# Kernel tuning notes

Hardware: AMD Instinct MI355X
Metric: run time of the kernel (lower is better)

Reference implementation:

```python
import jax, jax.numpy as jnp
import numpy as np

BN_EPS = 1e-5
NUM_GRAPHS = 64


def setup_inputs() -> dict:
    key = jax.random.key(0)
    ks = jax.random.split(key, 10)
    N, F, H, E = 50000, 128, 256, 800000
    x = jax.random.normal(ks[0], (N, F), dtype=jnp.float32)
    edge_index = jax.random.randint(ks[1], (2, E), 0, N, dtype=jnp.int64)
    batch = jnp.sort(jax.random.randint(ks[2], (N,), 0, NUM_GRAPHS, dtype=jnp.int64))
    # Linear weights stored as [in, out]; y = z @ w + b (equivalent to torch Linear)
    w1_0 = jax.random.normal(ks[3], (F, H), dtype=jnp.float32) / np.sqrt(F)
    b1_0 = jnp.zeros((H,), jnp.float32)
    w2_0 = jax.random.normal(ks[4], (H, H), dtype=jnp.float32) / np.sqrt(H)
    b2_0 = jnp.zeros((H,), jnp.float32)
    g_0 = jnp.ones((H,), jnp.float32)
    be_0 = jnp.zeros((H,), jnp.float32)
    w1_r = jax.random.normal(ks[5], (3, H, H), dtype=jnp.float32) / np.sqrt(H)
    b1_r = jnp.zeros((3, H), jnp.float32)
    w2_r = jax.random.normal(ks[6], (3, H, H), dtype=jnp.float32) / np.sqrt(H)
    b2_r = jnp.zeros((3, H), jnp.float32)
    g_r = jnp.ones((3, H), jnp.float32)
    be_r = jnp.zeros((3, H), jnp.float32)
    return dict(x=x, edge_index=edge_index, batch=batch,
                w1_0=w1_0, b1_0=b1_0, w2_0=w2_0, b2_0=b2_0, g_0=g_0, be_0=be_0,
                w1_r=w1_r, b1_r=b1_r, w2_r=w2_r, b2_r=b2_r, g_r=g_r, be_r=be_r)


def _gin_layer(h, src, dst, n, w1, b1, w2, b2, g, be):
    # GINConv with eps=0: MLP(h_i + sum_{j->i} h_j), scatter-add over edges
    agg = jax.ops.segment_sum(h[src], dst, num_segments=n)  # [N, d]
    z = agg + h
    z = jnp.maximum(z @ w1 + b1, 0.0)
    z = z @ w2 + b2
    # BatchNorm1d over the node dimension (training-mode batch statistics)
    mu = jnp.mean(z, axis=0)
    var = jnp.var(z, axis=0)
    z = (z - mu) * jax.lax.rsqrt(var + BN_EPS) * g + be
    return jnp.maximum(z, 0.0)  # ReLU; dropout is identity in eval mode


def reference(x, edge_index, batch, w1_0, b1_0, w2_0, b2_0, g_0, be_0,
              w1_r, b1_r, w2_r, b2_r, g_r, be_r):
    src, dst = edge_index[0], edge_index[1]
    n = x.shape[0]
    h = _gin_layer(x, src, dst, n, w1_0, b1_0, w2_0, b2_0, g_0, be_0)
    for i in range(3):
        h = _gin_layer(h, src, dst, n, w1_r[i], b1_r[i], w2_r[i], b2_r[i], g_r[i], be_r[i])
    # global mean pool per graph id
    counts = jax.ops.segment_sum(jnp.ones((n,), h.dtype), batch, num_segments=NUM_GRAPHS)
    pooled = jax.ops.segment_sum(h, batch, num_segments=NUM_GRAPHS)
    return pooled / jnp.maximum(counts, 1.0)[:, None]
```

## Files before the change

kernel.cpp:

```cpp
#include <hip/hip_runtime.h>

typedef float  f32x4 __attribute__((ext_vector_type(4)));
typedef _Float16 half8 __attribute__((ext_vector_type(8)));
typedef _Float16 half4 __attribute__((ext_vector_type(4)));

#define BN_EPS 1e-5f
#define NGRAPH 64

struct PrepArgs {
    const float* src[8];
    _Float16*    dst[8];
    int          K[8];
};

__global__ void prep_weights(PrepArgs a) {
    int m = blockIdx.y;
    int K = a.K[m];
    int total = K << 8;
    int idx = blockIdx.x * blockDim.x + threadIdx.x;
    if (idx >= total) return;
    int n = idx / K;
    int k = idx - n * K;
    a.dst[m][idx] = (_Float16)a.src[m][(size_t)k * 256 + n];
}

__global__ void edge_count(const int* __restrict__ ei, int* __restrict__ cnt,
                           int* __restrict__ rank, int E) {
    int e = blockIdx.x * blockDim.x + threadIdx.x;
    if (e < E) rank[e] = atomicAdd(&cnt[ei[E + e]], 1);
}

__global__ void scan_p1(const int* __restrict__ cnt, int* __restrict__ part, int N) {
    __shared__ int lds[256];
    int idx = blockIdx.x * 256 + threadIdx.x;
    lds[threadIdx.x] = (idx < N) ? cnt[idx] : 0;
    __syncthreads();
    for (int d = 128; d > 0; d >>= 1) {
        if (threadIdx.x < d) lds[threadIdx.x] += lds[threadIdx.x + d];
        __syncthreads();
    }
    if (threadIdx.x == 0) part[blockIdx.x] = lds[0];
}

__global__ void scan_p2(int* __restrict__ part, int* __restrict__ off, int N, int nb) {
    __shared__ int lds[256];
    int t = threadIdx.x;
    int v = (t < nb) ? part[t] : 0;
    lds[t] = v;
    __syncthreads();
    for (int d = 1; d < 256; d <<= 1) {
        int a = (t >= d) ? lds[t - d] : 0;
        __syncthreads();
        lds[t] += a;
        __syncthreads();
    }
    if (t < nb) part[t] = lds[t] - v;
    if (t == nb - 1) off[N] = lds[t];
}

__global__ void scan_p3(const int* __restrict__ cnt, const int* __restrict__ part,
                        int* __restrict__ off, int N) {
    __shared__ int lds[256];
    int t = threadIdx.x;
    int idx = blockIdx.x * 256 + t;
    int v = (idx < N) ? cnt[idx] : 0;
    lds[t] = v;
    __syncthreads();
    for (int d = 1; d < 256; d <<= 1) {
        int a = (t >= d) ? lds[t - d] : 0;
        __syncthreads();
        lds[t] += a;
        __syncthreads();
    }
    if (idx < N) off[idx] = part[blockIdx.x] + lds[t] - v;
}

__global__ void edge_fill(const int* __restrict__ ei, const int* __restrict__ off,
                          const int* __restrict__ rank, int* __restrict__ csr_src, int E) {
    int e = blockIdx.x * blockDim.x + threadIdx.x;
    if (e >= E) return;
    csr_src[off[ei[E + e]] + rank[e]] = ei[e];
}

__global__ void gather_f32(const float* __restrict__ x, const int* __restrict__ off,
                           const int* __restrict__ srcs, _Float16* __restrict__ out, int N) {
    int wid = (blockIdx.x << 2) + (threadIdx.x >> 6);
    if (wid >= N) return;
    int lane = threadIdx.x & 63;
    int half = lane >> 5;
    int fb = (lane & 31) << 2;
    float acc[4] = {0.f, 0.f, 0.f, 0.f};
    int beg = off[wid], end = off[wid + 1];
    int e = beg + half;
    for (; e + 2 < end; e += 4) {
        int s0 = srcs[e], s1 = srcs[e + 2];
        f32x4 v0 = *(const f32x4*)(x + (size_t)s0 * 128 + fb);
        f32x4 v1 = *(const f32x4*)(x + (size_t)s1 * 128 + fb);
#pragma unroll
        for (int k = 0; k < 4; ++k) acc[k] += v0[k] + v1[k];
    }
    if (e < end) {
        int s0 = srcs[e];
        f32x4 v0 = *(const f32x4*)(x + (size_t)s0 * 128 + fb);
#pragma unroll
        for (int k = 0; k < 4; ++k) acc[k] += v0[k];
    }
    if (half == 0) {
        f32x4 v = *(const f32x4*)(x + (size_t)wid * 128 + fb);
#pragma unroll
        for (int k = 0; k < 4; ++k) acc[k] += v[k];
    }
#pragma unroll
    for (int k = 0; k < 4; ++k) acc[k] += __shfl_xor(acc[k], 32);
    if (half == 0) {
        half4 o;
#pragma unroll
        for (int k = 0; k < 4; ++k) o[k] = (_Float16)acc[k];
        *(half4*)(out + (size_t)wid * 128 + fb) = o;
    }
}

__global__ void gather_fused(const _Float16* __restrict__ z, const int* __restrict__ off,
                             const int* __restrict__ srcs, const float* __restrict__ stats,
                             const float* __restrict__ gam, const float* __restrict__ bet,
                             _Float16* __restrict__ out, int N, float invN) {
    int wid = (blockIdx.x << 2) + (threadIdx.x >> 6);
    if (wid >= N) return;
    int lane = threadIdx.x & 63;
    int half = lane >> 5;
    int fb = (lane & 31) << 3;
    float sc[8], tc[8];
#pragma unroll
    for (int k = 0; k < 8; ++k) {
        float mu = stats[fb + k] * invN;
        float var = stats[256 + fb + k] * invN - mu * mu;
        float s = gam[fb + k] * rsqrtf(var + BN_EPS);
        sc[k] = s;
        tc[k] = bet[fb + k] - mu * s;
    }
    float acc[8] = {0.f, 0.f, 0.f, 0.f, 0.f, 0.f, 0.f, 0.f};
    int beg = off[wid], end = off[wid + 1];
    int e = beg + half;
    for (; e + 2 < end; e += 4) {
        int s0 = srcs[e], s1 = srcs[e + 2];
        half8 v0 = *(const half8*)(z + (size_t)s0 * 256 + fb);
        half8 v1 = *(const half8*)(z + (size_t)s1 * 256 + fb);
#pragma unroll
        for (int k = 0; k < 8; ++k)
            acc[k] += fmaxf(fmaf((float)v0[k], sc[k], tc[k]), 0.f)
                    + fmaxf(fmaf((float)v1[k], sc[k], tc[k]), 0.f);
    }
    if (e < end) {
        int s0 = srcs[e];
        half8 v0 = *(const half8*)(z + (size_t)s0 * 256 + fb);
#pragma unroll
        for (int k = 0; k < 8; ++k)
            acc[k] += fmaxf(fmaf((float)v0[k], sc[k], tc[k]), 0.f);
    }
    if (half == 0) {
        half8 v = *(const half8*)(z + (size_t)wid * 256 + fb);
#pragma unroll
        for (int k = 0; k < 8; ++k)
            acc[k] += fmaxf(fmaf((float)v[k], sc[k], tc[k]), 0.f);
    }
#pragma unroll
    for (int k = 0; k < 8; ++k) acc[k] += __shfl_xor(acc[k], 32);
    if (half == 0) {
        half8 o;
#pragma unroll
        for (int k = 0; k < 8; ++k) o[k] = (_Float16)acc[k];
        *(half8*)(out + (size_t)wid * 256 + fb) = o;
    }
}

template <int K, int WITH_STATS>
__global__ __launch_bounds__(512, 2) void gemm_kernel(
    const _Float16* __restrict__ A, const _Float16* __restrict__ BT,
    const float* __restrict__ bias, _Float16* __restrict__ Y,
    _Float16* __restrict__ Z, float* __restrict__ stats, int M) {
    extern __shared__ _Float16 blds[];
    const int tid = threadIdx.x;
    const int colbase = blockIdx.y * 128;
    {
        int row = tid >> 2;
        int q = tid & 3;
        int kq = q * (K / 4);
        const _Float16* src = BT + (size_t)(colbase + row) * K + kq;
        _Float16* dst = blds + row * K;
        int sw = (row & 7) << 3;
#pragma unroll
        for (int c = 0; c < K / 4; c += 8)
            *(half8*)(dst + ((kq + c) ^ sw)) = *(const half8*)(src + c);
    }
    __syncthreads();

    const int lane = tid & 63;
    const int wave = tid >> 6;
    const int i = lane & 15;
    const int g = lane >> 4;
    const int rowbase = blockIdx.x * 128 + wave * 16;
    const int arow = min(rowbase + i, M - 1);

    half8 afrag[K / 32];
#pragma unroll
    for (int s = 0; s < K / 32; ++s)
        afrag[s] = *(const half8*)(A + (size_t)arow * K + s * 32 + g * 8);

    f32x4 acc[8];
#pragma unroll
    for (int t = 0; t < 8; ++t) acc[t] = (f32x4){0.f, 0.f, 0.f, 0.f};

    const int sw = (i & 7) << 3;
#pragma unroll
    for (int s = 0; s < K / 32; ++s) {
#pragma unroll
        for (int t = 0; t < 8; ++t) {
            half8 b = *(const half8*)(blds + (t * 16 + i) * K + ((s * 32 + g * 8) ^ sw));
            acc[t] = __builtin_amdgcn_mfma_f32_16x16x32_f16(afrag[s], b, acc[t], 0, 0, 0);
        }
    }

    const int rg = g * 4;
    if (WITH_STATS == 0) {
#pragma unroll
        for (int t = 0; t < 8; ++t) {
            int c = colbase + t * 16 + i;
            float bv = bias[c];
#pragma unroll
            for (int j = 0; j < 4; ++j) {
                int r = rowbase + rg + j;
                if (r < M) Y[(size_t)r * 256 + c] = (_Float16)fmaxf(acc[t][j] + bv, 0.f);
            }
        }
    } else {
        float* sred = (float*)blds;
        __syncthreads();
#pragma unroll
        for (int t = 0; t < 8; ++t) {
            int c = colbase + t * 16 + i;
            float bv = bias[c];
            float s1 = 0.f, s2 = 0.f;
#pragma unroll
            for (int j = 0; j < 4; ++j) {
                int r = rowbase + rg + j;
                if (r < M) {
                    float v = acc[t][j] + bv;
                    Z[(size_t)r * 256 + c] = (_Float16)v;
                    s1 += v;
                    s2 += v * v;
                }
            }
            s1 += __shfl_xor(s1, 16); s1 += __shfl_xor(s1, 32);
            s2 += __shfl_xor(s2, 16); s2 += __shfl_xor(s2, 32);
            if (g == 0) {
                sred[wave * 128 + t * 16 + i] = s1;
                sred[1024 + wave * 128 + t * 16 + i] = s2;
            }
        }
        __syncthreads();
        if (tid < 256) {
            int which = tid >> 7;
            int c = tid & 127;
            float s = 0.f;
#pragma unroll
            for (int w = 0; w < 8; ++w) s += sred[which * 1024 + w * 128 + c];
            atomicAdd(&stats[which * 256 + colbase + c], s);
        }
    }
}

__global__ void graph_bounds(const int* __restrict__ batch, int* __restrict__ gstart, int N) {
    int t = threadIdx.x;
    if (t > NGRAPH) return;
    if (t == NGRAPH) { gstart[t] = N; return; }
    int lo = 0, hi = N;
    while (lo < hi) { int m = (lo + hi) >> 1; if (batch[m] < t) lo = m + 1; else hi = m; }
    gstart[t] = lo;
}

#define PCHUNK 256
__global__ void pool_stage1(const _Float16* __restrict__ z, const int* __restrict__ batch,
                            const int* __restrict__ gstart, const float* __restrict__ stats,
                            const float* __restrict__ gam, const float* __restrict__ bet,
                            float* __restrict__ acc, int N, float invN) {
    __shared__ float lds[8 * 512];
    int c0 = blockIdx.x * PCHUNK;
    int cend = min(c0 + PCHUNK, N);
    int tid = threadIdx.x;
    int rowlane = tid >> 5;
    int fb = (tid & 31) << 3;
    float sc[8], tc[8];
#pragma unroll
    for (int k = 0; k < 8; ++k) {
        float mu = stats[fb + k] * invN;
        float var = stats[256 + fb + k] * invN - mu * mu;
        float s = gam[fb + k] * rsqrtf(var + BN_EPS);
        sc[k] = s;
        tc[k] = bet[fb + k] - mu * s;
    }
    int segs = c0;
    while (segs < cend) {
        int g = batch[segs];
        int sege = min(gstart[g + 1], cend);
        float a[8] = {0.f, 0.f, 0.f, 0.f, 0.f, 0.f, 0.f, 0.f};
        for (int r = segs + rowlane; r < sege; r += 16) {
            half8 v = *(const half8*)(z + (size_t)r * 256 + fb);
#pragma unroll
            for (int k = 0; k < 8; ++k)
                a[k] += fmaxf(fmaf((float)v[k], sc[k], tc[k]), 0.f);
        }
#pragma unroll
        for (int k = 0; k < 8; ++k) lds[k * 512 + tid] = a[k];
        __syncthreads();
#pragma unroll
        for (int d = 8; d > 0; d >>= 1) {
            if (rowlane < d) {
#pragma unroll
                for (int k = 0; k < 8; ++k)
                    lds[k * 512 + tid] += lds[k * 512 + tid + d * 32];
            }
            __syncthreads();
        }
        if (rowlane == 0) {
#pragma unroll
            for (int k = 0; k < 8; ++k)
                atomicAdd(&acc[g * 256 + fb + k], lds[k * 512 + tid]);
        }
        __syncthreads();
        segs = sege;
    }
}

__global__ void pool_finalize(const float* __restrict__ acc, const int* __restrict__ gstart,
                              float* __restrict__ out) {
    int i = blockIdx.x * 256 + threadIdx.x;
    int g = i >> 8;
    int c = gstart[g + 1] - gstart[g];
    out[i] = acc[i] / (float)(c > 0 ? c : 1);
}

extern "C" void kernel_launch(void* const* d_in, const int* in_sizes, int n_in,
                              void* d_out, int out_size, void* d_ws, size_t ws_size,
                              hipStream_t stream) {
    const float* x    = (const float*)d_in[0];
    const int*   ei   = (const int*)d_in[1];
    const int*   batch= (const int*)d_in[2];
    const float* w1_0 = (const float*)d_in[3];
    const float* b1_0 = (const float*)d_in[4];
    const float* w2_0 = (const float*)d_in[5];
    const float* b2_0 = (const float*)d_in[6];
    const float* g_0  = (const float*)d_in[7];
    const float* be_0 = (const float*)d_in[8];
    const float* w1_r = (const float*)d_in[9];
    const float* b1_r = (const float*)d_in[10];
    const float* w2_r = (const float*)d_in[11];
    const float* b2_r = (const float*)d_in[12];
    const float* g_r  = (const float*)d_in[13];
    const float* be_r = (const float*)d_in[14];

    const int N = in_sizes[0] / 128;
    const int E = in_sizes[1] / 2;

    char* p = (char*)d_ws;
    auto alloc = [&](size_t bytes) { char* r = p; p += (bytes + 255) & ~(size_t)255; return r; };
    float*    stats   = (float*)alloc(4 * 512 * sizeof(float));
    int*      part    = (int*)alloc(256 * sizeof(int));
    int*      off     = (int*)alloc((size_t)(N + 1) * sizeof(int));
    int*      cnt     = (int*)alloc((size_t)N * sizeof(int));
    int*      gstart  = (int*)alloc(65 * sizeof(int));
    float*    acc     = (float*)alloc(NGRAPH * 256 * sizeof(float));
    int*      rank    = (int*)alloc((size_t)E * sizeof(int));
    int*      csr_src = (int*)alloc((size_t)E * sizeof(int));
    _Float16* wT      = (_Float16*)alloc((size_t)491520 * sizeof(_Float16));
    _Float16* zin     = (_Float16*)alloc((size_t)N * 256 * sizeof(_Float16));
    _Float16* y       = (_Float16*)alloc((size_t)N * 256 * sizeof(_Float16));
    _Float16* z       = (_Float16*)alloc((size_t)N * 256 * sizeof(_Float16));

    hipMemsetAsync(stats, 0, 4 * 512 * sizeof(float), stream);
    hipMemsetAsync(cnt, 0, (size_t)N * sizeof(int), stream);
    hipMemsetAsync(acc, 0, NGRAPH * 256 * sizeof(float), stream);

    PrepArgs pa;
    pa.src[0] = w1_0;  pa.dst[0] = wT;           pa.K[0] = 128;
    pa.src[1] = w2_0;  pa.dst[1] = wT + 32768;   pa.K[1] = 256;
    for (int i = 0; i < 3; ++i) {
        pa.src[2 + i] = w1_r + (size_t)i * 65536; pa.dst[2 + i] = wT + 98304 + (size_t)i * 65536; pa.K[2 + i] = 256;
        pa.src[5 + i] = w2_r + (size_t)i * 65536; pa.dst[5 + i] = wT + 294912 + (size_t)i * 65536; pa.K[5 + i] = 256;
    }
    prep_weights<<<dim3(256, 8), 256, 0, stream>>>(pa);

    const int eb = (E + 255) / 256;
    const int nb = (N + 255) / 256;
    edge_count<<<eb, 256, 0, stream>>>(ei, cnt, rank, E);
    scan_p1<<<nb, 256, 0, stream>>>(cnt, part, N);
    scan_p2<<<1, 256, 0, stream>>>(part, off, N, nb);
    scan_p3<<<nb, 256, 0, stream>>>(cnt, part, off, N);
    edge_fill<<<eb, 256, 0, stream>>>(ei, off, rank, csr_src, E);
    graph_bounds<<<1, 128, 0, stream>>>(batch, gstart, N);

    const int gwb   = (N + 3) / 4;
    const dim3 gemmg((N + 127) / 128, 2);
    const float invN = 1.0f / (float)N;

    gather_f32<<<gwb, 256, 0, stream>>>(x, off, csr_src, zin, N);
    gemm_kernel<128, 0><<<gemmg, 512, 128 * 128 * 2, stream>>>(zin, wT, b1_0, y, nullptr, nullptr, N);
    gemm_kernel<256, 1><<<gemmg, 512, 128 * 256 * 2, stream>>>(y, wT + 32768, b2_0, nullptr, z, stats, N);

    const float* cur_stats = stats;
    const float* cur_g = g_0;
    const float* cur_be = be_0;
    for (int i = 0; i < 3; ++i) {
        gather_fused<<<gwb, 256, 0, stream>>>(z, off, csr_src, cur_stats, cur_g, cur_be, zin, N, invN);
        gemm_kernel<256, 0><<<gemmg, 512, 128 * 256 * 2, stream>>>(
            zin, wT + 98304 + (size_t)i * 65536, b1_r + i * 256, y, nullptr, nullptr, N);
        gemm_kernel<256, 1><<<gemmg, 512, 128 * 256 * 2, stream>>>(
            y, wT + 294912 + (size_t)i * 65536, b2_r + i * 256, nullptr, z, stats + (i + 1) * 512, N);
        cur_stats = stats + (i + 1) * 512;
        cur_g = g_r + i * 256;
        cur_be = be_r + i * 256;
    }

    pool_stage1<<<(N + PCHUNK - 1) / PCHUNK, 512, 0, stream>>>(
        z, batch, gstart, cur_stats, cur_g, cur_be, acc, N, invN);
    pool_finalize<<<NGRAPH, 256, 0, stream>>>(acc, gstart, (float*)d_out);
}
```

Before: 576.1 us.

## Fuse both MLP GEMMs per layer, cast input to fp16, use packed half BN

Replaces the two separate GEMM launches per layer with one kernel. It computes the first GEMM into LDS, applies bias and ReLU there, then does the second GEMM reading W2 straight from global memory, which removes the round trip of the intermediate y through HBM. Input x is cast to fp16 once so the first gather reads half the bytes. The fused gather's BN+ReLU now runs in packed fp16 with deeper unrolling. Risks include lower fp16 precision in the BN transform, W2 fragments reloaded from global or L2 by every wave, and 1024-thread blocks using 128KB of LDS, which limits occupancy.

```diff
diff --git a/kernel.cpp b/kernel.cpp
--- a/kernel.cpp
+++ b/kernel.cpp
@@ -24,6 +24,17 @@
     a.dst[m][idx] = (_Float16)a.src[m][(size_t)k * 256 + n];
 }
 
+__global__ void cast_x(const float* __restrict__ x, _Float16* __restrict__ o, int total) {
+    int i = (blockIdx.x * blockDim.x + threadIdx.x) << 3;
+    if (i >= total) return;
+    f32x4 a = *(const f32x4*)(x + i);
+    f32x4 b = *(const f32x4*)(x + i + 4);
+    half8 r;
+#pragma unroll
+    for (int k = 0; k < 4; ++k) { r[k] = (_Float16)a[k]; r[k + 4] = (_Float16)b[k]; }
+    *(half8*)(o + i) = r;
+}
+
 __global__ void edge_count(const int* __restrict__ ei, int* __restrict__ cnt,
                            int* __restrict__ rank, int E) {
     int e = blockIdx.x * blockDim.x + threadIdx.x;
@@ -82,41 +93,44 @@
     csr_src[off[ei[E + e]] + rank[e]] = ei[e];
 }
 
-__global__ void gather_f32(const float* __restrict__ x, const int* __restrict__ off,
-                           const int* __restrict__ srcs, _Float16* __restrict__ out, int N) {
+__global__ void gather0(const _Float16* __restrict__ x, const int* __restrict__ off,
+                        const int* __restrict__ srcs, _Float16* __restrict__ out, int N) {
     int wid = (blockIdx.x << 2) + (threadIdx.x >> 6);
     if (wid >= N) return;
     int lane = threadIdx.x & 63;
-    int half = lane >> 5;
-    int fb = (lane & 31) << 2;
-    float acc[4] = {0.f, 0.f, 0.f, 0.f};
-    int beg = off[wid], end = off[wid + 1];
-    int e = beg + half;
-    for (; e + 2 < end; e += 4) {
-        int s0 = srcs[e], s1 = srcs[e + 2];
-        f32x4 v0 = *(const f32x4*)(x + (size_t)s0 * 128 + fb);
-        f32x4 v1 = *(const f32x4*)(x + (size_t)s1 * 128 + fb);
-#pragma unroll
-        for (int k = 0; k < 4; ++k) acc[k] += v0[k] + v1[k];
+    int q = lane >> 4;
+    int fb = (lane & 15) << 3;
+    float acc[8] = {0.f, 0.f, 0.f, 0.f, 0.f, 0.f, 0.f, 0.f};
+    int end = off[wid + 1];
+    int e = off[wid] + q;
+    for (; e + 4 < end; e += 8) {
+        int s0 = srcs[e], s1 = srcs[e + 4];
+        half8 v0 = *(const half8*)(x + (size_t)s0 * 128 + fb);
+        half8 v1 = *(const half8*)(x + (size_t)s1 * 128 + fb);
+#pragma unroll
+        for (int k = 0; k < 8; ++k) acc[k] += (float)v0[k] + (float)v1[k];
     }
     if (e < end) {
         int s0 = srcs[e];
-        f32x4 v0 = *(const f32x4*)(x + (size_t)s0 * 128 + fb);
-#pragma unroll
-        for (int k = 0; k < 4; ++k) acc[k] += v0[k];
-    }
-    if (half == 0) {
-        f32x4 v = *(const f32x4*)(x + (size_t)wid * 128 + fb);
-#pragma unroll
-        for (int k = 0; k < 4; ++k) acc[k] += v[k];
-    }
-#pragma unroll
-    for (int k = 0; k < 4; ++k) acc[k] += __shfl_xor(acc[k], 32);
-    if (half == 0) {
-        half4 o;
-#pragma unroll
-        for (int k = 0; k < 4; ++k) o[k] = (_Float16)acc[k];
-        *(half4*)(out + (size_t)wid * 128 + fb) = o;
+        half8 v0 = *(const half8*)(x + (size_t)s0 * 128 + fb);
+#pragma unroll
+        for (int k = 0; k < 8; ++k) acc[k] += (float)v0[k];
+    }
+    if (q == 0) {
+        half8 v = *(const half8*)(x + (size_t)wid * 128 + fb);
+#pragma unroll
+        for (int k = 0; k < 8; ++k) acc[k] += (float)v[k];
+    }
+#pragma unroll
+    for (int k = 0; k < 8; ++k) {
+        acc[k] += __shfl_xor(acc[k], 16);
+        acc[k] += __shfl_xor(acc[k], 32);
+    }
+    if (q == 0) {
+        half8 o;
+#pragma unroll
+        for (int k = 0; k < 8; ++k) o[k] = (_Float16)acc[k];
+        *(half8*)(out + (size_t)wid * 128 + fb) = o;
     }
 }
 
@@ -127,45 +141,51 @@
     int wid = (blockIdx.x << 2) + (threadIdx.x >> 6);
     if (wid >= N) return;
     int lane = threadIdx.x & 63;
-    int half = lane >> 5;
+    int hf = lane >> 5;
     int fb = (lane & 31) << 3;
-    float sc[8], tc[8];
+    half8 sc8, tc8;
 #pragma unroll
     for (int k = 0; k < 8; ++k) {
         float mu = stats[fb + k] * invN;
         float var = stats[256 + fb + k] * invN - mu * mu;
         float s = gam[fb + k] * rsqrtf(var + BN_EPS);
-        sc[k] = s;
-        tc[k] = bet[fb + k] - mu * s;
-    }
+        sc8[k] = (_Float16)s;
+        tc8[k] = (_Float16)(bet[fb + k] - mu * s);
+    }
+    const half8 zero8 = {0, 0, 0, 0, 0, 0, 0, 0};
     float acc[8] = {0.f, 0.f, 0.f, 0.f, 0.f, 0.f, 0.f, 0.f};
-    int beg = off[wid], end = off[wid + 1];
-    int e = beg + half;
-    for (; e + 2 < end; e += 4) {
-        int s0 = srcs[e], s1 = srcs[e + 2];
+    int end = off[wid + 1];
+    int e = off[wid] + hf;
+    for (; e + 6 < end; e += 8) {
+        int s0 = srcs[e], s1 = srcs[e + 2], s2 = srcs[e + 4], s3 = srcs[e + 6];
         half8 v0 = *(const half8*)(z + (size_t)s0 * 256 + fb);
         half8 v1 = *(const half8*)(z + (size_t)s1 * 256 + fb);
+        half8 v2 = *(const half8*)(z + (size_t)s2 * 256 + fb);
+        half8 v3 = *(const half8*)(z + (size_t)s3 * 256 + fb);
+        half8 r0 = __builtin_elementwise_max(v0 * sc8 + tc8, zero8);
+        half8 r1 = __builtin_elementwise_max(v1 * sc8 + tc8, zero8);
+        half8 r2 = __builtin_elementwise_max(v2 * sc8 + tc8, zero8);
+        half8 r3 = __builtin_elementwise_max(v3 * sc8 + tc8, zero8);
 #pragma unroll
         for (int k = 0; k < 8; ++k)
-            acc[k] += fmaxf(fmaf((float)v0[k], sc[k], tc[k]), 0.f)
-                    + fmaxf(fmaf((float)v1[k], sc[k], tc[k]), 0.f);
-    }
-    if (e < end) {
+            acc[k] += ((float)r0[k] + (float)r1[k]) + ((float)r2[k] + (float)r3[k]);
+    }
+    for (; e < end; e += 2) {
         int s0 = srcs[e];
         half8 v0 = *(const half8*)(z + (size_t)s0 * 256 + fb);
-#pragma unroll
-        for (int k = 0; k < 8; ++k)
-            acc[k] += fmaxf(fmaf((float)v0[k], sc[k], tc[k]), 0.f);
-    }
-    if (half == 0) {
+        half8 r0 = __builtin_elementwise_max(v0 * sc8 + tc8, zero8);
+#pragma unroll
+        for (int k = 0; k < 8; ++k) acc[k] += (float)r0[k];
+    }
+    if (hf == 0) {
         half8 v = *(const half8*)(z + (size_t)wid * 256 + fb);
-#pragma unroll
-        for (int k = 0; k < 8; ++k)
-            acc[k] += fmaxf(fmaf((float)v[k], sc[k], tc[k]), 0.f);
+        half8 r = __builtin_elementwise_max(v * sc8 + tc8, zero8);
+#pragma unroll
+        for (int k = 0; k < 8; ++k) acc[k] += (float)r[k];
     }
 #pragma unroll
     for (int k = 0; k < 8; ++k) acc[k] += __shfl_xor(acc[k], 32);
-    if (half == 0) {
+    if (hf == 0) {
         half8 o;
 #pragma unroll
         for (int k = 0; k < 8; ++k) o[k] = (_Float16)acc[k];
@@ -173,99 +193,104 @@
     }
 }
 
-template <int K, int WITH_STATS>
-__global__ __launch_bounds__(512, 2) void gemm_kernel(
-    const _Float16* __restrict__ A, const _Float16* __restrict__ BT,
-    const float* __restrict__ bias, _Float16* __restrict__ Y,
-    _Float16* __restrict__ Z, float* __restrict__ stats, int M) {
-    extern __shared__ _Float16 blds[];
+template <int K1>
+__global__ __launch_bounds__(1024) void mlp_fused(
+    const _Float16* __restrict__ A, const _Float16* __restrict__ W1T,
+    const float* __restrict__ b1, const _Float16* __restrict__ W2T,
+    const float* __restrict__ b2, _Float16* __restrict__ Z,
+    float* __restrict__ stats, int M) {
+    extern __shared__ _Float16 lds[];
     const int tid = threadIdx.x;
-    const int colbase = blockIdx.y * 128;
+    const int lane = tid & 63, wave = tid >> 6;
+    const int i = lane & 15, g = lane >> 4;
+    const int rowbase = blockIdx.x * 256 + wave * 16;
+    const int arow = min(rowbase + i, M - 1);
+
+    half8 afrag[K1 / 32];
+#pragma unroll
+    for (int s = 0; s < K1 / 32; ++s)
+        afrag[s] = *(const half8*)(A + (size_t)arow * K1 + s * 32 + g * 8);
+
     {
-        int row = tid >> 2;
-        int q = tid & 3;
-        int kq = q * (K / 4);
-        const _Float16* src = BT + (size_t)(colbase + row) * K + kq;
-        _Float16* dst = blds + row * K;
+        int row = tid >> 2, q = tid & 3, kq = q * (K1 / 4);
+        const _Float16* src = W1T + (size_t)row * K1 + kq;
+        _Float16* dst = lds + row * K1;
         int sw = (row & 7) << 3;
 #pragma unroll
-        for (int c = 0; c < K / 4; c += 8)
+        for (int c = 0; c < K1 / 4; c += 8)
             *(half8*)(dst + ((kq + c) ^ sw)) = *(const half8*)(src + c);
     }
     __syncthreads();
 
-    const int lane = tid & 63;
-    const int wave = tid >> 6;
-    const int i = lane & 15;
-    const int g = lane >> 4;
-    const int rowbase = blockIdx.x * 128 + wave * 16;
-    const int arow = min(rowbase + i, M - 1);
-
-    half8 afrag[K / 32];
-#pragma unroll
-    for (int s = 0; s < K / 32; ++s)
-        afrag[s] = *(const half8*)(A + (size_t)arow * K + s * 32 + g * 8);
-
-    f32x4 acc[8];
-#pragma unroll
-    for (int t = 0; t < 8; ++t) acc[t] = (f32x4){0.f, 0.f, 0.f, 0.f};
-
-    const int sw = (i & 7) << 3;
-#pragma unroll
-    for (int s = 0; s < K / 32; ++s) {
-#pragma unroll
-        for (int t = 0; t < 8; ++t) {
-            half8 b = *(const half8*)(blds + (t * 16 + i) * K + ((s * 32 + g * 8) ^ sw));
+    const int swi = (i & 7) << 3;
+    f32x4 acc[16];
+#pragma unroll
+    for (int t = 0; t < 16; ++t) acc[t] = (f32x4){0.f, 0.f, 0.f, 0.f};
+#pragma unroll
+    for (int t = 0; t < 16; ++t)
+#pragma unroll
+        for (int s = 0; s < K1 / 32; ++s) {
+            half8 b = *(const half8*)(lds + (t * 16 + i) * K1 + ((s * 32 + g * 8) ^ swi));
             acc[t] = __builtin_amdgcn_mfma_f32_16x16x32_f16(afrag[s], b, acc[t], 0, 0, 0);
         }
-    }
-
-    const int rg = g * 4;
-    if (WITH_STATS == 0) {
-#pragma unroll
-        for (int t = 0; t < 8; ++t) {
-            int c = colbase + t * 16 + i;
-            float bv = bias[c];
-#pragma unroll
-            for (int j = 0; j < 4; ++j) {
-                int r = rowbase + rg + j;
-                if (r < M) Y[(size_t)r * 256 + c] = (_Float16)fmaxf(acc[t][j] + bv, 0.f);
+    __syncthreads();
+
+#pragma unroll
+    for (int t = 0; t < 16; ++t) {
+        int c = t * 16 + i;
+        float bv = b1[c];
+#pragma unroll
+        for (int j = 0; j < 4; ++j) {
+            int r = wave * 16 + g * 4 + j;
+            lds[r * 256 + (c ^ ((r & 7) << 3))] = (_Float16)fmaxf(acc[t][j] + bv, 0.f);
+        }
+    }
+    __syncthreads();
+
+#pragma unroll
+    for (int t = 0; t < 16; ++t) acc[t] = (f32x4){0.f, 0.f, 0.f, 0.f};
+    const int yrow = wave * 16 + i;
+#pragma unroll
+    for (int s = 0; s < 8; ++s) {
+        half8 yf = *(const half8*)(lds + yrow * 256 + ((s * 32 + g * 8) ^ swi));
+#pragma unroll
+        for (int t = 0; t < 16; ++t) {
+            half8 wf = *(const half8*)(W2T + (size_t)(t * 16 + i) * 256 + s * 32 + g * 8);
+            acc[t] = __builtin_amdgcn_mfma_f32_16x16x32_f16(yf, wf, acc[t], 0, 0, 0);
+        }
+    }
+    __syncthreads();
+
+    float* sred = (float*)lds;
+#pragma unroll
+    for (int t = 0; t < 16; ++t) {
+        int c = t * 16 + i;
+        float bv = b2[c];
+        float s1 = 0.f, s2 = 0.f;
+#pragma unroll
+        for (int j = 0; j < 4; ++j) {
+            int r = rowbase + g * 4 + j;
+            if (r < M) {
+                float v = acc[t][j] + bv;
+                Z[(size_t)r * 256 + c] = (_Float16)v;
+                s1 += v;
+                s2 += v * v;
             }
         }
-    } else {
-        float* sred = (float*)blds;
-        __syncthreads();
-#pragma unroll
-        for (int t = 0; t < 8; ++t) {
-            int c = colbase + t * 16 + i;
-            float bv = bias[c];
-            float s1 = 0.f, s2 = 0.f;
-#pragma unroll
-            for (int j = 0; j < 4; ++j) {
-                int r = rowbase + rg + j;
-                if (r < M) {
-                    float v = acc[t][j] + bv;
-                    Z[(size_t)r * 256 + c] = (_Float16)v;
-                    s1 += v;
-                    s2 += v * v;
-                }
-            }
-            s1 += __shfl_xor(s1, 16); s1 += __shfl_xor(s1, 32);
-            s2 += __shfl_xor(s2, 16); s2 += __shfl_xor(s2, 32);
-            if (g == 0) {
-                sred[wave * 128 + t * 16 + i] = s1;
-                sred[1024 + wave * 128 + t * 16 + i] = s2;
-            }
-        }
-        __syncthreads();
-        if (tid < 256) {
-            int which = tid >> 7;
-            int c = tid & 127;
-            float s = 0.f;
-#pragma unroll
-            for (int w = 0; w < 8; ++w) s += sred[which * 1024 + w * 128 + c];
-            atomicAdd(&stats[which * 256 + colbase + c], s);
-        }
+        s1 += __shfl_xor(s1, 16); s1 += __shfl_xor(s1, 32);
+        s2 += __shfl_xor(s2, 16); s2 += __shfl_xor(s2, 32);
+        if (g == 0) {
+            sred[wave * 256 + c] = s1;
+            sred[4096 + wave * 256 + c] = s2;
+        }
+    }
+    __syncthreads();
+    if (tid < 512) {
+        int which = tid >> 8, c = tid & 255;
+        float s = 0.f;
+#pragma unroll
+        for (int w = 0; w < 16; ++w) s += sred[which * 4096 + w * 256 + c];
+        atomicAdd(&stats[which * 256 + c], s);
     }
 }
 
@@ -368,17 +393,17 @@
     int*      off     = (int*)alloc((size_t)(N + 1) * sizeof(int));
     int*      cnt     = (int*)alloc((size_t)N * sizeof(int));
     int*      gstart  = (int*)alloc(65 * sizeof(int));
-    float*    acc     = (float*)alloc(NGRAPH * 256 * sizeof(float));
+    float*    accp    = (float*)alloc(NGRAPH * 256 * sizeof(float));
     int*      rank    = (int*)alloc((size_t)E * sizeof(int));
     int*      csr_src = (int*)alloc((size_t)E * sizeof(int));
     _Float16* wT      = (_Float16*)alloc((size_t)491520 * sizeof(_Float16));
+    _Float16* x16     = (_Float16*)alloc((size_t)N * 128 * sizeof(_Float16));
     _Float16* zin     = (_Float16*)alloc((size_t)N * 256 * sizeof(_Float16));
-    _Float16* y       = (_Float16*)alloc((size_t)N * 256 * sizeof(_Float16));
     _Float16* z       = (_Float16*)alloc((size_t)N * 256 * sizeof(_Float16));
 
     hipMemsetAsync(stats, 0, 4 * 512 * sizeof(float), stream);
     hipMemsetAsync(cnt, 0, (size_t)N * sizeof(int), stream);
-    hipMemsetAsync(acc, 0, NGRAPH * 256 * sizeof(float), stream);
+    hipMemsetAsync(accp, 0, NGRAPH * 256 * sizeof(float), stream);
 
     PrepArgs pa;
     pa.src[0] = w1_0;  pa.dst[0] = wT;           pa.K[0] = 128;
@@ -388,6 +413,7 @@
         pa.src[5 + i] = w2_r + (size_t)i * 65536; pa.dst[5 + i] = wT + 294912 + (size_t)i * 65536; pa.K[5 + i] = 256;
     }
     prep_weights<<<dim3(256, 8), 256, 0, stream>>>(pa);
+    cast_x<<<(N * 128 / 8 + 255) / 256, 256, 0, stream>>>(x, x16, N * 128);
 
     const int eb = (E + 255) / 256;
     const int nb = (N + 255) / 256;
@@ -398,29 +424,27 @@
     edge_fill<<<eb, 256, 0, stream>>>(ei, off, rank, csr_src, E);
     graph_bounds<<<1, 128, 0, stream>>>(batch, gstart, N);
 
-    const int gwb   = (N + 3) / 4;
-    const dim3 gemmg((N + 127) / 128, 2);
+    const int gwb = (N + 3) / 4;
+    const int mlpg = (N + 255) / 256;
     const float invN = 1.0f / (float)N;
 
-    gather_f32<<<gwb, 256, 0, stream>>>(x, off, csr_src, zin, N);
-    gemm_kernel<128, 0><<<gemmg, 512, 128 * 128 * 2, stream>>>(zin, wT, b1_0, y, nullptr, nullptr, N);
-    gemm_kernel<256, 1><<<gemmg, 512, 128 * 256 * 2, stream>>>(y, wT + 32768, b2_0, nullptr, z, stats, N);
+    gather0<<<gwb, 256, 0, stream>>>(x16, off, csr_src, zin, N);
+    mlp_fused<128><<<mlpg, 1024, 131072, stream>>>(zin, wT, b1_0, wT + 32768, b2_0, z, stats, N);
 
     const float* cur_stats = stats;
     const float* cur_g = g_0;
     const float* cur_be = be_0;
     for (int i = 0; i < 3; ++i) {
         gather_fused<<<gwb, 256, 0, stream>>>(z, off, csr_src, cur_stats, cur_g, cur_be, zin, N, invN);
-        gemm_kernel<256, 0><<<gemmg, 512, 128 * 256 * 2, stream>>>(
-            zin, wT + 98304 + (size_t)i * 65536, b1_r + i * 256, y, nullptr, nullptr, N);
-        gemm_kernel<256, 1><<<gemmg, 512, 128 * 256 * 2, stream>>>(
-            y, wT + 294912 + (size_t)i * 65536, b2_r + i * 256, nullptr, z, stats + (i + 1) * 512, N);
+        mlp_fused<256><<<mlpg, 1024, 131072, stream>>>(
+            zin, wT + 98304 + (size_t)i * 65536, b1_r + i * 256,
+            wT + 294912 + (size_t)i * 65536, b2_r + i * 256, z, stats + (i + 1) * 512, N);
         cur_stats = stats + (i + 1) * 512;
         cur_g = g_r + i * 256;
         cur_be = be_r + i * 256;
     }
 
     pool_stage1<<<(N + PCHUNK - 1) / PCHUNK, 512, 0, stream>>>(
-        z, batch, gstart, cur_stats, cur_g, cur_be, acc, N, invN);
-    pool_finalize<<<NGRAPH, 256, 0, stream>>>(acc, gstart, (float*)d_out);
-}
+        z, batch, gstart, cur_stats, cur_g, cur_be, accp, N, invN);
+    pool_finalize<<<NGRAPH, 256, 0, stream>>>(accp, gstart, (float*)d_out);
+}
```

After: 658.2 us. 14.3% more time.
